# Optimization experiments

Measured on AMD Instinct MI355X. Metric: run time of the kernel, lower is better.

## Reference

```python
import jax, jax.numpy as jnp
import numpy as np

B, T, D = 32, 2048, 1024


def setup_inputs() -> dict:
    key = jax.random.key(0)
    k1, k2, k3, k4, k5, k6 = jax.random.split(key, 6)
    return {
        "keys": jax.random.normal(k1, (B, T, D), dtype=jnp.float32),
        "value": jax.random.normal(k2, (B, T, D), dtype=jnp.float32),
        "query": jax.random.normal(k3, (B, D), dtype=jnp.float32),
        "weight_feedback": jax.random.normal(k4, (B, T, D), dtype=jnp.float32),
        "v": jax.random.normal(k5, (D,), dtype=jnp.float32) / np.sqrt(D),
        "enc_seq_len": jax.random.randint(k6, (B,), 1, T + 1, dtype=jnp.int32),
    }


def reference(keys, value, query, weight_feedback, v, enc_seq_len):
    # energies = v^T tanh(key + query + weight_feedback)  -> [B, T]
    hidden = jnp.tanh(keys + query[:, None, :] + weight_feedback)  # [B,T,D]
    energies = jnp.einsum("btd,d->bt", hidden, v)                  # [B,T]
    # length mask + softmax over time
    mask = jnp.arange(energies.shape[1])[None, :] < enc_seq_len[:, None]  # [B,T]
    energies = jnp.where(mask, energies, -jnp.inf)
    weights = jax.nn.softmax(energies, axis=1)                      # [B,T]
    # context = weights^T value -> [B, D_v]
    context = jnp.einsum("bt,btd->bd", weights, value)
    return context, weights[:, :, None]
```

## Files before the change

kernel.cpp:

```cpp
#include <hip/hip_runtime.h>
#include <math.h>

#define BB 32
#define TT 2048
#define DD 1024
#define TCHUNK 64

__device__ __forceinline__ float fast_tanh(float x) {
    float e = __expf(2.0f * x);
    return 1.0f - __fdividef(2.0f, e + 1.0f);
}

__global__ __launch_bounds__(256) void energies_kernel(
    const float* __restrict__ keys, const float* __restrict__ query,
    const float* __restrict__ wf, const float* __restrict__ v,
    const int* __restrict__ lenp, float* __restrict__ eout)
{
    const int t = blockIdx.x;
    const int b = blockIdx.y;
    if (t >= lenp[b]) return;

    const int d = threadIdx.x * 4;
    const size_t row = ((size_t)b * TT + t) * DD;

    const float4 k4 = *(const float4*)(keys + row + d);
    const float4 w4 = *(const float4*)(wf   + row + d);
    const float4 q4 = *(const float4*)(query + (size_t)b * DD + d);
    const float4 v4 = *(const float4*)(v + d);

    float s = fast_tanh(k4.x + q4.x + w4.x) * v4.x
            + fast_tanh(k4.y + q4.y + w4.y) * v4.y
            + fast_tanh(k4.z + q4.z + w4.z) * v4.z
            + fast_tanh(k4.w + q4.w + w4.w) * v4.w;

    #pragma unroll
    for (int off = 32; off > 0; off >>= 1) s += __shfl_down(s, off, 64);
    __shared__ float red[4];
    if ((threadIdx.x & 63) == 0) red[threadIdx.x >> 6] = s;
    __syncthreads();
    if (threadIdx.x == 0)
        eout[(size_t)b * TT + t] = red[0] + red[1] + red[2] + red[3];
}

__global__ __launch_bounds__(256) void softmax_kernel(
    const int* __restrict__ lenp, float* __restrict__ wrow_all)
{
    const int b = blockIdx.x;
    const int L = lenp[b];
    float* wrow = wrow_all + (size_t)b * TT;

    float e[8];
    float m = -INFINITY;
    #pragma unroll
    for (int i = 0; i < 8; i++) {
        const int t = threadIdx.x + i * 256;
        e[i] = (t < L) ? wrow[t] : -INFINITY;
        m = fmaxf(m, e[i]);
    }
    #pragma unroll
    for (int off = 1; off < 64; off <<= 1) m = fmaxf(m, __shfl_xor(m, off, 64));
    __shared__ float redm[4];
    const int wv = threadIdx.x >> 6;
    if ((threadIdx.x & 63) == 0) redm[wv] = m;
    __syncthreads();
    m = fmaxf(fmaxf(redm[0], redm[1]), fmaxf(redm[2], redm[3]));

    float s = 0.0f;
    #pragma unroll
    for (int i = 0; i < 8; i++) {
        e[i] = (e[i] == -INFINITY) ? 0.0f : __expf(e[i] - m);
        s += e[i];
    }
    #pragma unroll
    for (int off = 1; off < 64; off <<= 1) s += __shfl_xor(s, off, 64);
    __shared__ float reds[4];
    if ((threadIdx.x & 63) == 0) reds[wv] = s;
    __syncthreads();
    s = reds[0] + reds[1] + reds[2] + reds[3];
    const float inv = 1.0f / s;

    #pragma unroll
    for (int i = 0; i < 8; i++)
        wrow[threadIdx.x + i * 256] = e[i] * inv;
}

__global__ __launch_bounds__(256) void context_kernel(
    const float* __restrict__ value, const float* __restrict__ weights,
    const int* __restrict__ lenp, float* __restrict__ context)
{
    const int b = blockIdx.y;
    const int L = lenp[b];
    const int t0 = blockIdx.x * TCHUNK;
    if (t0 >= L) return;
    const int tend = min(t0 + TCHUNK, L);
    const int d = threadIdx.x * 4;

    float4 acc = make_float4(0.f, 0.f, 0.f, 0.f);
    for (int t = t0; t < tend; t++) {
        const float w = weights[(size_t)b * TT + t];
        const float4 v4 = *(const float4*)(value + ((size_t)b * TT + t) * DD + d);
        acc.x += w * v4.x; acc.y += w * v4.y;
        acc.z += w * v4.z; acc.w += w * v4.w;
    }
    float* dst = context + (size_t)b * DD + d;
    atomicAdd(dst + 0, acc.x);
    atomicAdd(dst + 1, acc.y);
    atomicAdd(dst + 2, acc.z);
    atomicAdd(dst + 3, acc.w);
}

extern "C" void kernel_launch(void* const* d_in, const int* in_sizes, int n_in,
                              void* d_out, int out_size, void* d_ws, size_t ws_size,
                              hipStream_t stream) {
    const float* keys  = (const float*)d_in[0];
    const float* value = (const float*)d_in[1];
    const float* query = (const float*)d_in[2];
    const float* wf    = (const float*)d_in[3];
    const float* v     = (const float*)d_in[4];
    const int*   lenp  = (const int*)d_in[5];

    float* out      = (float*)d_out;
    float* context  = out;
    float* weights  = out + BB * DD;

    hipMemsetAsync(context, 0, (size_t)BB * DD * sizeof(float), stream);

    energies_kernel<<<dim3(TT, BB), 256, 0, stream>>>(keys, query, wf, v, lenp, weights);
    softmax_kernel<<<BB, 256, 0, stream>>>(lenp, weights);
    context_kernel<<<dim3(TT / TCHUNK, BB), 256, 0, stream>>>(value, weights, lenp, context);
}
```

Measured before the change: 596.0 us.

## Map one wave per time row in energies, fold memset into softmax, cache weights

The energies kernel now assigns one 64-lane wave to each time row, four rows per block, with a loop over four float4 chunks. This removes the shared-memory reduction and block barrier and cuts the launch to a quarter of the blocks. The context buffer is zeroed inside the softmax kernel instead of by a separate memset. The context kernel stages its chunk of weights in shared memory. The aim is to reduce per-block and launch overhead on a bandwidth-bound workload.

```diff
diff --git a/kernel.cpp b/kernel.cpp
--- a/kernel.cpp
+++ b/kernel.cpp
@@ -16,38 +16,44 @@
     const float* __restrict__ wf, const float* __restrict__ v,
     const int* __restrict__ lenp, float* __restrict__ eout)
 {
-    const int t = blockIdx.x;
-    const int b = blockIdx.y;
+    const int b    = blockIdx.y;
+    const int wave = threadIdx.x >> 6;
+    const int lane = threadIdx.x & 63;
+    const int t    = blockIdx.x * 4 + wave;
     if (t >= lenp[b]) return;
 
-    const int d = threadIdx.x * 4;
-    const size_t row = ((size_t)b * TT + t) * DD;
+    const size_t row  = ((size_t)b * TT + t) * DD;
+    const size_t qrow = (size_t)b * DD;
 
-    const float4 k4 = *(const float4*)(keys + row + d);
-    const float4 w4 = *(const float4*)(wf   + row + d);
-    const float4 q4 = *(const float4*)(query + (size_t)b * DD + d);
-    const float4 v4 = *(const float4*)(v + d);
-
-    float s = fast_tanh(k4.x + q4.x + w4.x) * v4.x
-            + fast_tanh(k4.y + q4.y + w4.y) * v4.y
-            + fast_tanh(k4.z + q4.z + w4.z) * v4.z
-            + fast_tanh(k4.w + q4.w + w4.w) * v4.w;
-
+    float s = 0.0f;
+    #pragma unroll
+    for (int k = 0; k < 4; k++) {
+        const int d = k * 256 + lane * 4;
+        const float4 k4 = *(const float4*)(keys + row + d);
+        const float4 w4 = *(const float4*)(wf   + row + d);
+        const float4 q4 = *(const float4*)(query + qrow + d);
+        const float4 v4 = *(const float4*)(v + d);
+        s += fast_tanh(k4.x + q4.x + w4.x) * v4.x
+           + fast_tanh(k4.y + q4.y + w4.y) * v4.y
+           + fast_tanh(k4.z + q4.z + w4.z) * v4.z
+           + fast_tanh(k4.w + q4.w + w4.w) * v4.w;
+    }
     #pragma unroll
     for (int off = 32; off > 0; off >>= 1) s += __shfl_down(s, off, 64);
-    __shared__ float red[4];
-    if ((threadIdx.x & 63) == 0) red[threadIdx.x >> 6] = s;
-    __syncthreads();
-    if (threadIdx.x == 0)
-        eout[(size_t)b * TT + t] = red[0] + red[1] + red[2] + red[3];
+    if (lane == 0) eout[(size_t)b * TT + t] = s;
 }
 
 __global__ __launch_bounds__(256) void softmax_kernel(
-    const int* __restrict__ lenp, float* __restrict__ wrow_all)
+    const int* __restrict__ lenp, float* __restrict__ wrow_all,
+    float* __restrict__ context)
 {
     const int b = blockIdx.x;
     const int L = lenp[b];
     float* wrow = wrow_all + (size_t)b * TT;
+
+    #pragma unroll
+    for (int i = 0; i < 4; i++)
+        context[(size_t)b * DD + threadIdx.x + i * 256] = 0.0f;
 
     float e[8];
     float m = -INFINITY;
@@ -95,9 +101,15 @@
     const int tend = min(t0 + TCHUNK, L);
     const int d = threadIdx.x * 4;
 
+    __shared__ float wsh[TCHUNK];
+    if (threadIdx.x < TCHUNK)
+        wsh[threadIdx.x] = weights[(size_t)b * TT + t0 + threadIdx.x];
+    __syncthreads();
+
     float4 acc = make_float4(0.f, 0.f, 0.f, 0.f);
+    #pragma unroll 2
     for (int t = t0; t < tend; t++) {
-        const float w = weights[(size_t)b * TT + t];
+        const float w = wsh[t - t0];
         const float4 v4 = *(const float4*)(value + ((size_t)b * TT + t) * DD + d);
         acc.x += w * v4.x; acc.y += w * v4.y;
         acc.z += w * v4.z; acc.w += w * v4.w;
@@ -123,9 +135,7 @@
     float* context  = out;
     float* weights  = out + BB * DD;
 
-    hipMemsetAsync(context, 0, (size_t)BB * DD * sizeof(float), stream);
-
-    energies_kernel<<<dim3(TT, BB), 256, 0, stream>>>(keys, query, wf, v, lenp, weights);
-    softmax_kernel<<<BB, 256, 0, stream>>>(lenp, weights);
+    energies_kernel<<<dim3(TT / 4, BB), 256, 0, stream>>>(keys, query, wf, v, lenp, weights);
+    softmax_kernel<<<BB, 256, 0, stream>>>(lenp, weights, context);
     context_kernel<<<dim3(TT / TCHUNK, BB), 256, 0, stream>>>(value, weights, lenp, context);
 }
```

After: 596.6 us. Within noise of the previous version (+0.1%).
